# Optimization experiments

Hardware: AMD Instinct MI355X
Metric: run time of the kernel (lower is better)

## Reference

```python
import jax, jax.numpy as jnp
import numpy as np

HEADS, DIM_HEAD, INNER, DIM = 6, 50, 300, 768
HW, EXTRA, POOL = 100, 150, 10  # spatial side, extra tokens, pool output side
N = HW * HW + EXTRA  # 10150


def setup_inputs() -> dict:
    key = jax.random.key(0)
    ks = jax.random.split(key, 6)
    B = 8
    x = jax.random.normal(ks[0], (B, N, DIM), dtype=jnp.float32)
    # weights scaled ~ typical init so softmax logits are sane
    proj_w = jax.random.normal(ks[1], (INNER, DIM), dtype=jnp.float32) * 0.02
    step_x = jax.random.normal(ks[2], (HEADS, 1, 1), dtype=jnp.float32)
    step_rep = jax.random.normal(ks[3], (HEADS, 1, 1), dtype=jnp.float32)
    out_w = jax.random.normal(ks[4], (DIM, INNER), dtype=jnp.float32) * 0.02
    out_b = jax.random.normal(ks[5], (DIM,), dtype=jnp.float32) * 0.02
    return {"x": x, "proj_w": proj_w, "step_x": step_x, "step_rep": step_rep,
            "out_w": out_w, "out_b": out_b}


def reference(x, proj_w, step_x, step_rep, out_w, out_b):
    b, n, c = x.shape
    hw = int(round((n - EXTRA) ** 0.5))
    scale = DIM_HEAD ** -0.5

    w = x @ proj_w.T  # [b, n, 300]

    # adaptive avg pool of the spatial tokens to (10,10); hw % 10 == 0 -> uniform pooling
    k = hw // POOL
    spatial = w[:, : hw * hw, :].reshape(b, hw, hw, INNER).transpose(0, 3, 1, 2)  # [b,300,hw,hw]
    rep = spatial.reshape(b, INNER, POOL, k, POOL, k).mean(axis=(3, 5))  # [b,300,10,10]
    rep = rep.reshape(b, INNER, POOL * POOL).transpose(0, 2, 1)  # [b,100,300]

    wh = w.reshape(b, n, HEADS, DIM_HEAD).transpose(0, 2, 1, 3)        # [b,h,n,d]
    reph = rep.reshape(b, POOL * POOL, HEADS, DIM_HEAD).transpose(0, 2, 1, 3)  # [b,h,100,d]

    # stage 1: rep attends to all tokens
    dots = jnp.einsum('bhqd,bhkd->bhqk', reph, wh) * scale  # [b,h,100,n]
    attn = jax.nn.softmax(dots, axis=-1)
    rep_delta = jnp.einsum('bhqk,bhkd->bhqd', attn, wh)     # [b,h,100,d]
    reph = reph + step_rep * rep_delta

    # stage 2: rep self-attention, broadcast back through reused attn^T
    dots2 = jnp.einsum('bhqd,bhkd->bhqk', reph, reph) * scale  # [b,h,100,100]
    attn2 = jax.nn.softmax(dots2, axis=-1)
    x_delta = jnp.einsum('bhqk,bhkd->bhqd', attn2, reph)       # [b,h,100,d]
    x_delta = jnp.einsum('bhqn,bhqd->bhnd', attn, x_delta)     # attn^T @ x_delta -> [b,h,n,d]
    x_delta = step_x * x_delta

    x_delta = x_delta.transpose(0, 2, 1, 3).reshape(b, n, HEADS * DIM_HEAD)  # [b,n,300]
    return x_delta @ out_w.T + out_b
```

## Files before the change

kernel.cpp:

```cpp
#include <hip/hip_runtime.h>
#include <math.h>

#define BATCH   8
#define NTOK    10150
#define DIMC    768
#define INNERC  300
#define HEADS   6
#define DHEAD   50
#define NQ      100
#define NBH     48
#define NSPLIT  32
#define CHUNK   320
#define SCALE   0.14142135623730951f
#define MTOT    (BATCH*NTOK)
#define XDK     320
#define NEGBIG  -1.0e30f
#define LDS_S   44

typedef __attribute__((ext_vector_type(8))) short short8;
typedef __attribute__((ext_vector_type(4))) float f32x4;

__device__ __forceinline__ ushort f2bf(float x) {
  uint u = __float_as_uint(x);
  uint r = (u + 0x7fffu + ((u >> 16) & 1u)) >> 16;
  return (ushort)r;
}
__device__ __forceinline__ float bf2f(ushort h) {
  return __uint_as_float(((uint)h) << 16);
}

__global__ void split_pad(const float* __restrict__ src, ushort* __restrict__ dHi,
                          ushort* __restrict__ dLo, int R, int C, int Rp, int Cp) {
  const int total = Rp * Cp;
  for (int i = blockIdx.x * blockDim.x + threadIdx.x; i < total;
       i += gridDim.x * blockDim.x) {
    const int r = i / Cp, c = i % Cp;
    const float v = (r < R && c < C) ? src[r * C + c] : 0.f;
    const ushort hh = f2bf(v);
    dHi[i] = hh;
    dLo[i] = f2bf(v - bf2f(hh));
  }
}

__global__ void zero_xd_pad(ushort* __restrict__ xdHi, ushort* __restrict__ xdLo) {
  const int total = MTOT * 20;
  for (int i = blockIdx.x * blockDim.x + threadIdx.x; i < total;
       i += gridDim.x * blockDim.x) {
    const size_t g = (size_t)(i / 20) * XDK + 300 + (i % 20);
    xdHi[g] = 0;
    xdLo[g] = 0;
  }
}

__global__ __launch_bounds__(512, 2) void gemm1_xw(
    const float* __restrict__ x, const ushort* __restrict__ pwHi,
    const ushort* __restrict__ pwLo, ushort* __restrict__ wHi,
    ushort* __restrict__ wLo) {
  __shared__ ushort aH[64][LDS_S], aL[64][LDS_S];
  __shared__ ushort bH[320][LDS_S], bL[320][LDS_S];
  const int t = threadIdx.x;
  const int lane = t & 63, w = t >> 6;
  const int wr = w >> 2, wc = w & 3;
  const int l15 = lane & 15, l4 = lane >> 4;
  const int m0 = blockIdx.x * 64;
  const int arow = t >> 3, aq = (t & 7) * 4;

  f32x4 acc[2][5];
#pragma unroll
  for (int i = 0; i < 2; ++i)
#pragma unroll
    for (int j = 0; j < 5; ++j) acc[i][j] = (f32x4){0.f, 0.f, 0.f, 0.f};

  for (int k0 = 0; k0 < DIMC; k0 += 32) {
    __syncthreads();
    {
      const int m = m0 + arow;
      float4 v = make_float4(0.f, 0.f, 0.f, 0.f);
      if (m < MTOT) v = *(const float4*)&x[(size_t)m * DIMC + k0 + aq];
      ushort h0 = f2bf(v.x), h1 = f2bf(v.y), h2 = f2bf(v.z), h3 = f2bf(v.w);
      *(ushort4*)&aH[arow][aq] = make_ushort4(h0, h1, h2, h3);
      *(ushort4*)&aL[arow][aq] = make_ushort4(
          f2bf(v.x - bf2f(h0)), f2bf(v.y - bf2f(h1)),
          f2bf(v.z - bf2f(h2)), f2bf(v.w - bf2f(h3)));
    }
#pragma unroll
    for (int i = 0; i < 3; ++i) {
      const int sid = t + i * 512;
      if (sid < 1280) {
        const int row = sid >> 2, slot = sid & 3;
        const size_t g = (size_t)row * DIMC + k0 + slot * 8;
        *(short8*)&bH[row][slot * 8] = *(const short8*)&pwHi[g];
        *(short8*)&bL[row][slot * 8] = *(const short8*)&pwLo[g];
      }
    }
    __syncthreads();

    short8 ah[2], al[2];
#pragma unroll
    for (int i = 0; i < 2; ++i) {
      const int row = wr * 32 + i * 16 + l15;
      ah[i] = *(const short8*)&aH[row][l4 * 8];
      al[i] = *(const short8*)&aL[row][l4 * 8];
    }
#pragma unroll
    for (int j = 0; j < 5; ++j) {
      const int brow = wc * 80 + j * 16 + l15;
      const short8 bhf = *(const short8*)&bH[brow][l4 * 8];
      const short8 blf = *(const short8*)&bL[brow][l4 * 8];
#pragma unroll
      for (int i = 0; i < 2; ++i) {
        acc[i][j] = __builtin_amdgcn_mfma_f32_16x16x32_bf16(ah[i], bhf, acc[i][j], 0, 0, 0);
        acc[i][j] = __builtin_amdgcn_mfma_f32_16x16x32_bf16(al[i], bhf, acc[i][j], 0, 0, 0);
        acc[i][j] = __builtin_amdgcn_mfma_f32_16x16x32_bf16(ah[i], blf, acc[i][j], 0, 0, 0);
      }
    }
  }

#pragma unroll
  for (int j = 0; j < 5; ++j) {
    const int col = wc * 80 + j * 16 + l15;
    if (col >= INNERC) continue;
#pragma unroll
    for (int i = 0; i < 2; ++i)
#pragma unroll
      for (int r = 0; r < 4; ++r) {
        const int m = m0 + wr * 32 + i * 16 + l4 * 4 + r;
        if (m < MTOT) {
          const float val = acc[i][j][r];
          const ushort hh = f2bf(val);
          const size_t g = (size_t)m * INNERC + col;
          wHi[g] = hh;
          wLo[g] = f2bf(val - bf2f(hh));
        }
      }
  }
}

__global__ __launch_bounds__(512, 2) void gemm2_out(
    const ushort* __restrict__ xdHi, const ushort* __restrict__ xdLo,
    const ushort* __restrict__ owHi, const ushort* __restrict__ owLo,
    const float* __restrict__ out_b, float* __restrict__ out) {
  __shared__ ushort aH[64][LDS_S], aL[64][LDS_S];
  __shared__ ushort bH[256][LDS_S], bL[256][LDS_S];
  const int t = threadIdx.x;
  const int lane = t & 63, w = t >> 6;
  const int wr = w >> 2, wc = w & 3;
  const int l15 = lane & 15, l4 = lane >> 4;
  const int nwg = gridDim.x;
  const int q = nwg >> 3, r = nwg & 7;
  const int xcd = blockIdx.x & 7, idx = blockIdx.x >> 3;
  const int wg = (xcd < r ? xcd * (q + 1) : r * (q + 1) + (xcd - r) * q) + idx;
  const int bn = wg % 3, bm = wg / 3;
  const int m0 = bm * 64, n0 = bn * 256;
  const int arow = t >> 3, aq = (t & 7) * 4;

  f32x4 acc[2][4];
#pragma unroll
  for (int i = 0; i < 2; ++i)
#pragma unroll
    for (int j = 0; j < 4; ++j) acc[i][j] = (f32x4){0.f, 0.f, 0.f, 0.f};

  for (int k0 = 0; k0 < XDK; k0 += 32) {
    __syncthreads();
    {
      const int m = m0 + arow;
      if (m < MTOT) {
        const size_t g = (size_t)m * XDK + k0 + aq;
        *(ushort4*)&aH[arow][aq] = *(const ushort4*)&xdHi[g];
        *(ushort4*)&aL[arow][aq] = *(const ushort4*)&xdLo[g];
      } else {
        *(ushort4*)&aH[arow][aq] = make_ushort4(0, 0, 0, 0);
        *(ushort4*)&aL[arow][aq] = make_ushort4(0, 0, 0, 0);
      }
    }
#pragma unroll
    for (int i = 0; i < 2; ++i) {
      const int sid = t + i * 512;
      const int row = sid >> 2, slot = sid & 3;
      const size_t g = (size_t)(n0 + row) * XDK + k0 + slot * 8;
      *(short8*)&bH[row][slot * 8] = *(const short8*)&owHi[g];
      *(short8*)&bL[row][slot * 8] = *(const short8*)&owLo[g];
    }
    __syncthreads();

    short8 ah[2], al[2];
#pragma unroll
    for (int i = 0; i < 2; ++i) {
      const int row = wr * 32 + i * 16 + l15;
      ah[i] = *(const short8*)&aH[row][l4 * 8];
      al[i] = *(const short8*)&aL[row][l4 * 8];
    }
#pragma unroll
    for (int j = 0; j < 4; ++j) {
      const int brow = wc * 64 + j * 16 + l15;
      const short8 bhf = *(const short8*)&bH[brow][l4 * 8];
      const short8 blf = *(const short8*)&bL[brow][l4 * 8];
#pragma unroll
      for (int i = 0; i < 2; ++i) {
        acc[i][j] = __builtin_amdgcn_mfma_f32_16x16x32_bf16(ah[i], bhf, acc[i][j], 0, 0, 0);
        acc[i][j] = __builtin_amdgcn_mfma_f32_16x16x32_bf16(al[i], bhf, acc[i][j], 0, 0, 0);
        acc[i][j] = __builtin_amdgcn_mfma_f32_16x16x32_bf16(ah[i], blf, acc[i][j], 0, 0, 0);
      }
    }
  }

#pragma unroll
  for (int j = 0; j < 4; ++j) {
    const int col = n0 + wc * 64 + j * 16 + l15;
    const float bv = out_b[col];
#pragma unroll
    for (int i = 0; i < 2; ++i)
#pragma unroll
      for (int r = 0; r < 4; ++r) {
        const int m = m0 + wr * 32 + i * 16 + l4 * 4 + r;
        if (m < MTOT) out[(size_t)m * DIMC + col] = acc[i][j][r] + bv;
      }
  }
}

__global__ void pool_kernel(const ushort* __restrict__ wHi,
                            const ushort* __restrict__ wLo,
                            float* __restrict__ rep,
                            ushort* __restrict__ repPH, ushort* __restrict__ repPL) {
  int q = blockIdx.x, b = blockIdx.y;
  int i = threadIdx.x;
  if (i < INNERC) {
    int pr = q / 10, pc = q % 10;
    float s = 0.f;
    for (int kr = 0; kr < 10; ++kr)
      for (int kc = 0; kc < 10; ++kc) {
        int tok = (pr * 10 + kr) * 100 + (pc * 10 + kc);
        const size_t g = ((size_t)b * NTOK + tok) * INNERC + i;
        s += bf2f(wHi[g]) + bf2f(wLo[g]);
      }
    s *= 0.01f;
    int h = i / DHEAD, d = i % DHEAD;
    rep[(((size_t)b * HEADS + h) * NQ + q) * DHEAD + d] = s;
    const float sv = s * SCALE;
    const ushort hh = f2bf(sv);
    const size_t pg = (((size_t)b * HEADS + h) * 128 + q) * 64 + d;
    repPH[pg] = hh;
    repPL[pg] = f2bf(sv - bf2f(hh));
  }
  for (int j = threadIdx.x; j < HEADS * 14; j += 320) {
    int h2 = j / 14, d2 = DHEAD + (j % 14);
    const size_t pg = (((size_t)b * HEADS + h2) * 128 + q) * 64 + d2;
    repPH[pg] = 0;
    repPL[pg] = 0;
  }
}

__global__ __launch_bounds__(256, 3) void attn1_mfma(
    const ushort* __restrict__ wHi, const ushort* __restrict__ wLo,
    const float* __restrict__ rep,
    float* __restrict__ m_part, float* __restrict__ l_part,
    float* __restrict__ delta_part) {
  const int bh = blockIdx.x, s = blockIdx.y;
  const int b = bh / HEADS, h = bh % HEADS;
  const int t = threadIdx.x;
  const int lane = t & 63, wv = t >> 6;
  const int l15 = lane & 15, l4 = lane >> 4;

  __shared__ ushort Khi[32][72], Klo[32][72];
  __shared__ ushort VThi[64][40], VTlo[64][40];
  __shared__ ushort Phi[128][40], Plo[128][40];

  short8 qhi[2][2], qlo[2][2];
#pragma unroll
  for (int mi = 0; mi < 2; ++mi) {
#pragma unroll
    for (int ks = 0; ks < 2; ++ks) {
      const int qr = 32 * wv + 16 * mi + l15;
      short8 th, tl;
#pragma unroll
      for (int j = 0; j < 8; ++j) {
        const int k = 32 * ks + 8 * l4 + j;
        float v = (qr < NQ && k < DHEAD)
                      ? rep[((size_t)bh * NQ + qr) * DHEAD + k] * SCALE : 0.f;
        ushort hh = f2bf(v);
        th[j] = (short)hh;
        tl[j] = (short)f2bf(v - bf2f(hh));
      }
      qhi[mi][ks] = th; qlo[mi][ks] = tl;
    }
  }

  f32x4 accO[2][4];
  float m_run[2][4], l_run[2][4];
#pragma unroll
  for (int mi = 0; mi < 2; ++mi) {
#pragma unroll
    for (int r = 0; r < 4; ++r) { m_run[mi][r] = NEGBIG; l_run[mi][r] = 0.f; }
#pragma unroll
    for (int di = 0; di < 4; ++di) accO[mi][di] = (f32x4){0.f, 0.f, 0.f, 0.f};
  }

  const int n0 = s * CHUNK;
  const int n1 = min(NTOK, n0 + CHUNK);

  for (int nt = n0; nt < n1; nt += 32) {
    __syncthreads();
#pragma unroll
    for (int i = 0; i < 4; ++i) {
      const int idx = t + i * 256;
      const int tr = idx >> 5;
      const int d = (idx & 31) * 2;
      const bool inb = (nt + tr < n1) && (d < DHEAD);
      uint hv = 0, lv = 0;
      if (inb) {
        const size_t g = ((size_t)b * NTOK + nt + tr) * INNERC + h * DHEAD + d;
        hv = *(const uint*)&wHi[g];
        lv = *(const uint*)&wLo[g];
      }
      *(uint*)&Khi[tr][d] = hv;
      *(uint*)&Klo[tr][d] = lv;
      const int ps = ((((tr >> 3) + (d >> 3)) & 3) << 3) + (tr & 7);
      VThi[d][ps] = (ushort)(hv & 0xffffu);
      VTlo[d][ps] = (ushort)(lv & 0xffffu);
      VThi[d + 1][ps] = (ushort)(hv >> 16);
      VTlo[d + 1][ps] = (ushort)(lv >> 16);
    }
    __syncthreads();

    f32x4 accS[2][2];
#pragma unroll
    for (int mi = 0; mi < 2; ++mi)
#pragma unroll
      for (int ni = 0; ni < 2; ++ni) accS[mi][ni] = (f32x4){0.f, 0.f, 0.f, 0.f};
#pragma unroll
    for (int ks = 0; ks < 2; ++ks) {
      short8 kh[2], kl[2];
#pragma unroll
      for (int ni = 0; ni < 2; ++ni) {
        kh[ni] = *(const short8*)&Khi[16 * ni + l15][32 * ks + 8 * l4];
        kl[ni] = *(const short8*)&Klo[16 * ni + l15][32 * ks + 8 * l4];
      }
#pragma unroll
      for (int mi = 0; mi < 2; ++mi)
#pragma unroll
        for (int ni = 0; ni < 2; ++ni) {
          accS[mi][ni] = __builtin_amdgcn_mfma_f32_16x16x32_bf16(qhi[mi][ks], kh[ni], accS[mi][ni], 0, 0, 0);
          accS[mi][ni] = __builtin_amdgcn_mfma_f32_16x16x32_bf16(qlo[mi][ks], kh[ni], accS[mi][ni], 0, 0, 0);
          accS[mi][ni] = __builtin_amdgcn_mfma_f32_16x16x32_bf16(qhi[mi][ks], kl[ni], accS[mi][ni], 0, 0, 0);
        }
    }

    bool cval[2];
#pragma unroll
    for (int ni = 0; ni < 2; ++ni) cval[ni] = (nt + 16 * ni + l15) < n1;
#pragma unroll
    for (int mi = 0; mi < 2; ++mi) {
#pragma unroll
      for (int ni = 0; ni < 2; ++ni)
        if (!cval[ni]) {
#pragma unroll
          for (int r = 0; r < 4; ++r) accS[mi][ni][r] = NEGBIG;
        }
#pragma unroll
      for (int r = 0; r < 4; ++r) {
        float mx = fmaxf(accS[mi][0][r], accS[mi][1][r]);
        mx = fmaxf(mx, __shfl_xor(mx, 1));
        mx = fmaxf(mx, __shfl_xor(mx, 2));
        mx = fmaxf(mx, __shfl_xor(mx, 4));
        mx = fmaxf(mx, __shfl_xor(mx, 8));
        const float m_new = fmaxf(m_run[mi][r], mx);
        const float sc = __expf(m_run[mi][r] - m_new);
        m_run[mi][r] = m_new;
        l_run[mi][r] *= sc;
#pragma unroll
        for (int di = 0; di < 4; ++di) accO[mi][di][r] *= sc;
        float ps = 0.f;
#pragma unroll
        for (int ni = 0; ni < 2; ++ni) {
          const float p = __expf(accS[mi][ni][r] - m_new);
          accS[mi][ni][r] = p;
          ps += p;
        }
        ps += __shfl_xor(ps, 1);
        ps += __shfl_xor(ps, 2);
        ps += __shfl_xor(ps, 4);
        ps += __shfl_xor(ps, 8);
        l_run[mi][r] += ps;
      }
#pragma unroll
      for (int ni = 0; ni < 2; ++ni)
#pragma unroll
        for (int r = 0; r < 4; ++r) {
          const int row = 32 * wv + 16 * mi + 4 * l4 + r;
          const int col = 16 * ni + l15;
          const float p = accS[mi][ni][r];
          const ushort ph = f2bf(p);
          Phi[row][col] = ph;
          Plo[row][col] = f2bf(p - bf2f(ph));
        }
    }

#pragma unroll
    for (int mi = 0; mi < 2; ++mi) {
      const short8 pah = *(const short8*)&Phi[32 * wv + 16 * mi + l15][8 * l4];
      const short8 pal = *(const short8*)&Plo[32 * wv + 16 * mi + l15][8 * l4];
#pragma unroll
      for (int di = 0; di < 4; ++di) {
        const int vs = (((l4 + 2 * di + (l15 >> 3)) & 3)) << 3;
        const short8 vbh = *(const short8*)&VThi[16 * di + l15][vs];
        const short8 vbl = *(const short8*)&VTlo[16 * di + l15][vs];
        accO[mi][di] = __builtin_amdgcn_mfma_f32_16x16x32_bf16(pah, vbh, accO[mi][di], 0, 0, 0);
        accO[mi][di] = __builtin_amdgcn_mfma_f32_16x16x32_bf16(pal, vbh, accO[mi][di], 0, 0, 0);
        accO[mi][di] = __builtin_amdgcn_mfma_f32_16x16x32_bf16(pah, vbl, accO[mi][di], 0, 0, 0);
      }
    }
  }

  const size_t base = ((size_t)bh * NSPLIT + s) * NQ;
#pragma unroll
  for (int mi = 0; mi < 2; ++mi)
#pragma unroll
    for (int r = 0; r < 4; ++r) {
      const int q = 32 * wv + 16 * mi + 4 * l4 + r;
      if (q < NQ && l15 == 0) {
        m_part[base + q] = m_run[mi][r];
        l_part[base + q] = l_run[mi][r];
      }
#pragma unroll
      for (int di = 0; di < 4; ++di) {
        const int d = 16 * di + l15;
        if (q < NQ && d < DHEAD)
          delta_part[(base + q) * DHEAD + d] = accO[mi][di][r];
      }
    }
}

__global__ __launch_bounds__(256) void attn1_combine(
    const float* __restrict__ rep, const float* __restrict__ m_part,
    const float* __restrict__ l_part, const float* __restrict__ delta_part,
    const float* __restrict__ step_rep,
    float* __restrict__ reph2, float* __restrict__ m_fin, float* __restrict__ l_fin) {
  int bh = blockIdx.x;
  int h = bh % HEADS;
  int t = threadIdx.x;
  __shared__ float Mf[NQ], Lf[NQ];
  if (t < NQ) {
    int q = t;
    float M = -INFINITY;
#pragma unroll
    for (int s2 = 0; s2 < NSPLIT; ++s2)
      M = fmaxf(M, m_part[((size_t)bh * NSPLIT + s2) * NQ + q]);
    float L = 0.f;
#pragma unroll
    for (int s2 = 0; s2 < NSPLIT; ++s2)
      L += l_part[((size_t)bh * NSPLIT + s2) * NQ + q] *
           __expf(m_part[((size_t)bh * NSPLIT + s2) * NQ + q] - M);
    Mf[q] = M; Lf[q] = L;
    m_fin[(size_t)bh * NQ + q] = M;
    l_fin[(size_t)bh * NQ + q] = L;
  }
  __syncthreads();
  float sr = step_rep[h];
  for (int idx = t; idx < NQ * DHEAD; idx += 256) {
    int q = idx / DHEAD, d = idx % DHEAD;
    float sum = 0.f;
#pragma unroll
    for (int s2 = 0; s2 < NSPLIT; ++s2) {
      size_t pb = ((size_t)bh * NSPLIT + s2) * NQ + q;
      sum += __expf(m_part[pb] - Mf[q]) * delta_part[pb * DHEAD + d];
    }
    float rd = sum / Lf[q];
    reph2[(size_t)bh * NQ * DHEAD + idx] =
        rep[(size_t)bh * NQ * DHEAD + idx] + sr * rd;
  }
}

__global__ __launch_bounds__(256) void attn2_kernel(
    const float* __restrict__ reph2, const float* __restrict__ step_x,
    ushort* __restrict__ xqTH, ushort* __restrict__ xqTL) {
  int bh = blockIdx.x;
  int h = bh % HEADS;
  int t = threadIdx.x;
  __shared__ float r2[NQ * DHEAD];
  __shared__ float att[NQ * NQ];

  for (int idx = t; idx < NQ * DHEAD; idx += 256)
    r2[idx] = reph2[(size_t)bh * NQ * DHEAD + idx];
  __syncthreads();

  for (int idx = t; idx < NQ * NQ; idx += 256) {
    int qq = idx / NQ, jj = idx % NQ;
    float s = 0.f;
#pragma unroll
    for (int k = 0; k < DHEAD; ++k) s += r2[qq * DHEAD + k] * r2[jj * DHEAD + k];
    att[idx] = s * SCALE;
  }
  __syncthreads();
  if (t < NQ) {
    float M = -INFINITY;
    for (int j = 0; j < NQ; ++j) M = fmaxf(M, att[t * NQ + j]);
    float L = 0.f;
    for (int j = 0; j < NQ; ++j) { float e = __expf(att[t * NQ + j] - M); att[t * NQ + j] = e; L += e; }
    float inv = 1.f / L;
    for (int j = 0; j < NQ; ++j) att[t * NQ + j] *= inv;
  }
  __syncthreads();
  float sx = step_x[h];
  for (int idx = t; idx < NQ * DHEAD; idx += 256) {
    int qd_q = idx / DHEAD, d = idx % DHEAD;
    float v = 0.f;
#pragma unroll
    for (int j = 0; j < NQ; ++j) v += att[qd_q * NQ + j] * r2[j * DHEAD + d];
    v *= sx;
    const size_t pg = ((size_t)bh * 64 + d) * 128 + qd_q;
    const ushort hh = f2bf(v);
    xqTH[pg] = hh;
    xqTL[pg] = f2bf(v - bf2f(hh));
  }
  for (int idx = t; idx < 64 * 28; idx += 256) {
    int d = idx / 28, qq2 = NQ + (idx % 28);
    const size_t pg = ((size_t)bh * 64 + d) * 128 + qq2;
    xqTH[pg] = 0;
    xqTL[pg] = 0;
  }
}

#define TT5 128
__global__ __launch_bounds__(256, 2) void bcast5_kernel(
    const ushort* __restrict__ wHi, const ushort* __restrict__ wLo,
    const ushort* __restrict__ repPH, const ushort* __restrict__ repPL,
    const ushort* __restrict__ xqTH, const ushort* __restrict__ xqTL,
    const float* __restrict__ m_fin, const float* __restrict__ l_fin,
    ushort* __restrict__ xdHi, ushort* __restrict__ xdLo) {
  const int tile = blockIdx.x, bh = blockIdx.y;
  const int b = bh / HEADS, h = bh % HEADS;
  const int tok0 = tile * TT5;
  const int t = threadIdx.x;
  const int lane = t & 63, wv = t >> 6;
  const int l15 = lane & 15, l4 = lane >> 4;

  __shared__ ushort pH[128][72], pL[128][72];

  short8 awh[2][2], awl[2][2];
#pragma unroll
  for (int st = 0; st < 2; ++st) {
    const int tokA = tok0 + st * 64 + 16 * wv + l15;
#pragma unroll
    for (int ks = 0; ks < 2; ++ks) {
      const int kbase = 32 * ks + 8 * l4;
      uint hv[4] = {0, 0, 0, 0}, lv[4] = {0, 0, 0, 0};
      if (tokA < NTOK && kbase < DHEAD) {
        const size_t g = ((size_t)b * NTOK + tokA) * INNERC + h * DHEAD + kbase;
#pragma unroll
        for (int c = 0; c < 4; ++c) {
          hv[c] = *(const uint*)&wHi[g + 2 * c];
          lv[c] = *(const uint*)&wLo[g + 2 * c];
        }
      }
      short8 th, tl;
#pragma unroll
      for (int j = 0; j < 8; ++j) {
        const bool ok = (kbase + j) < DHEAD;
        const ushort hsel = (j & 1) ? (ushort)(hv[j >> 1] >> 16) : (ushort)(hv[j >> 1] & 0xffffu);
        const ushort lsel = (j & 1) ? (ushort)(lv[j >> 1] >> 16) : (ushort)(lv[j >> 1] & 0xffffu);
        th[j] = ok ? (short)hsel : (short)0;
        tl[j] = ok ? (short)lsel : (short)0;
      }
      awh[st][ks] = th;
      awl[st][ks] = tl;
    }
  }

  f32x4 accO[2][4];
#pragma unroll
  for (int st = 0; st < 2; ++st)
#pragma unroll
    for (int di = 0; di < 4; ++di) accO[st][di] = (f32x4){0.f, 0.f, 0.f, 0.f};

#pragma unroll
  for (int qc = 0; qc < 2; ++qc) {
    const int q0 = qc * 64;

    short8 rbh[4][2], rbl[4][2];
#pragma unroll
    for (int ni = 0; ni < 4; ++ni)
#pragma unroll
      for (int ks = 0; ks < 2; ++ks) {
        const size_t rg = (((size_t)bh * 128) + (q0 + 16 * ni + l15)) * 64 + 32 * ks + 8 * l4;
        rbh[ni][ks] = *(const short8*)&repPH[rg];
        rbl[ni][ks] = *(const short8*)&repPL[rg];
      }
    float mq[4], li[4];
    bool vq[4];
#pragma unroll
    for (int ni = 0; ni < 4; ++ni) {
      const int q = q0 + 16 * ni + l15;
      vq[ni] = (q < NQ);
      mq[ni] = vq[ni] ? m_fin[(size_t)bh * NQ + q] : 0.f;
      li[ni] = vq[ni] ? 1.f / l_fin[(size_t)bh * NQ + q] : 0.f;
    }

#pragma unroll
    for (int st = 0; st < 2; ++st) {
      f32x4 accS[4];
#pragma unroll
      for (int ni = 0; ni < 4; ++ni) accS[ni] = (f32x4){0.f, 0.f, 0.f, 0.f};
#pragma unroll
      for (int ks = 0; ks < 2; ++ks)
#pragma unroll
        for (int ni = 0; ni < 4; ++ni) {
          accS[ni] = __builtin_amdgcn_mfma_f32_16x16x32_bf16(awh[st][ks], rbh[ni][ks], accS[ni], 0, 0, 0);
          accS[ni] = __builtin_amdgcn_mfma_f32_16x16x32_bf16(awl[st][ks], rbh[ni][ks], accS[ni], 0, 0, 0);
          accS[ni] = __builtin_amdgcn_mfma_f32_16x16x32_bf16(awh[st][ks], rbl[ni][ks], accS[ni], 0, 0, 0);
        }
#pragma unroll
      for (int ni = 0; ni < 4; ++ni) {
#pragma unroll
        for (int r = 0; r < 4; ++r) {
          const float p = vq[ni] ? __expf(accS[ni][r] - mq[ni]) * li[ni] : 0.f;
          const int row = st * 64 + 16 * wv + 4 * l4 + r;
          const ushort ph = f2bf(p);
          pH[row][16 * ni + l15] = ph;
          pL[row][16 * ni + l15] = f2bf(p - bf2f(ph));
        }
      }
    }

    short8 xbh[4][2], xbl[4][2];
#pragma unroll
    for (int di = 0; di < 4; ++di)
#pragma unroll
      for (int ks2 = 0; ks2 < 2; ++ks2) {
        const size_t xg = (((size_t)bh * 64) + (16 * di + l15)) * 128 + q0 + 32 * ks2 + 8 * l4;
        xbh[di][ks2] = *(const short8*)&xqTH[xg];
        xbl[di][ks2] = *(const short8*)&xqTL[xg];
      }

#pragma unroll
    for (int st = 0; st < 2; ++st) {
#pragma unroll
      for (int ks2 = 0; ks2 < 2; ++ks2) {
        const short8 pah = *(const short8*)&pH[st * 64 + 16 * wv + l15][32 * ks2 + 8 * l4];
        const short8 pal = *(const short8*)&pL[st * 64 + 16 * wv + l15][32 * ks2 + 8 * l4];
#pragma unroll
        for (int di = 0; di < 4; ++di) {
          accO[st][di] = __builtin_amdgcn_mfma_f32_16x16x32_bf16(pah, xbh[di][ks2], accO[st][di], 0, 0, 0);
          accO[st][di] = __builtin_amdgcn_mfma_f32_16x16x32_bf16(pal, xbh[di][ks2], accO[st][di], 0, 0, 0);
          accO[st][di] = __builtin_amdgcn_mfma_f32_16x16x32_bf16(pah, xbl[di][ks2], accO[st][di], 0, 0, 0);
        }
      }
    }
  }

#pragma unroll
  for (int st = 0; st < 2; ++st)
#pragma unroll
    for (int di = 0; di < 4; ++di) {
      const int d = di * 16 + l15;
      if (d >= DHEAD) continue;
#pragma unroll
      for (int r = 0; r < 4; ++r) {
        const int tok = tok0 + st * 64 + wv * 16 + 4 * l4 + r;
        if (tok < NTOK) {
          const float val = accO[st][di][r];
          const ushort hh = f2bf(val);
          const size_t g = ((size_t)b * NTOK + tok) * XDK + h * DHEAD + d;
          xdHi[g] = hh;
          xdLo[g] = f2bf(val - bf2f(hh));
        }
      }
    }
}

extern "C" void kernel_launch(void* const* d_in, const int* in_sizes, int n_in,
                              void* d_out, int out_size, void* d_ws, size_t ws_size,
                              hipStream_t stream) {
  const float* x        = (const float*)d_in[0];
  const float* proj_w   = (const float*)d_in[1];
  const float* step_x   = (const float*)d_in[2];
  const float* step_rep = (const float*)d_in[3];
  const float* out_w    = (const float*)d_in[4];
  const float* out_b    = (const float*)d_in[5];
  float* out = (float*)d_out;

  uint8_t* p8 = (uint8_t*)d_ws;
  ushort* wHi    = (ushort*)(p8);
  ushort* wLo    = (ushort*)(p8 + 48720000);
  float*  rep    = (float*) (p8 + 97440000);
  float*  reph2  = (float*) (p8 + 98400000);
  float*  m_part = (float*) (p8 + 100320000);
  float*  l_part = (float*) (p8 + 100934400);
  float*  m_fin  = (float*) (p8 + 101548800);
  float*  l_fin  = (float*) (p8 + 101568000);
  ushort* xdHi   = (ushort*)(p8 + 101587200);
  ushort* xdLo   = (ushort*)(p8 + 153555200);
  ushort* pwHi   = (ushort*)(p8 + 205523200);
  ushort* pwLo   = (ushort*)(p8 + 206014720);
  ushort* owHi   = (ushort*)(p8 + 206506240);
  ushort* owLo   = (ushort*)(p8 + 206997760);
  ushort* repPH  = (ushort*)(p8 + 207489280);
  ushort* repPL  = (ushort*)(p8 + 208275712);
  ushort* xqTH   = (ushort*)(p8 + 209062144);
  ushort* xqTL   = (ushort*)(p8 + 209848576);
  float* delta = (float*)xdHi;

  split_pad<<<960, 256, 0, stream>>>(proj_w, pwHi, pwLo, INNERC, DIMC, 320, DIMC);
  split_pad<<<960, 256, 0, stream>>>(out_w, owHi, owLo, DIMC, INNERC, DIMC, XDK);
  gemm1_xw<<<1269, 512, 0, stream>>>(x, pwHi, pwLo, wHi, wLo);
  pool_kernel<<<dim3(NQ, BATCH), 320, 0, stream>>>(wHi, wLo, rep, repPH, repPL);
  attn1_mfma<<<dim3(NBH, NSPLIT), 256, 0, stream>>>(wHi, wLo, rep, m_part, l_part, delta);
  attn1_combine<<<NBH, 256, 0, stream>>>(rep, m_part, l_part, delta, step_rep,
                                         reph2, m_fin, l_fin);
  zero_xd_pad<<<2048, 256, 0, stream>>>(xdHi, xdLo);
  attn2_kernel<<<NBH, 256, 0, stream>>>(reph2, step_x, xqTH, xqTL);
  bcast5_kernel<<<dim3(80, NBH), 256, 0, stream>>>(
      wHi, wLo, repPH, repPL, xqTH, xqTL, m_fin, l_fin, xdHi, xdLo);
  gemm2_out<<<3807, 512, 0, stream>>>(xdHi, xdLo, owHi, owLo, out_b, out);
}
```

Measured before the change: 778.4 us.

## Drop LDS staging in both GEMMs and load MFMA fragments directly from global

```diff
diff --git a/kernel.cpp b/kernel.cpp
--- a/kernel.cpp
+++ b/kernel.cpp
@@ -15,7 +15,6 @@
 #define MTOT    (BATCH*NTOK)
 #define XDK     320
 #define NEGBIG  -1.0e30f
-#define LDS_S   44
 
 typedef __attribute__((ext_vector_type(8))) short short8;
 typedef __attribute__((ext_vector_type(4))) float f32x4;
@@ -52,18 +51,15 @@
   }
 }
 
-__global__ __launch_bounds__(512, 2) void gemm1_xw(
+__global__ __launch_bounds__(512, 3) void gemm1_xw(
     const float* __restrict__ x, const ushort* __restrict__ pwHi,
     const ushort* __restrict__ pwLo, ushort* __restrict__ wHi,
     ushort* __restrict__ wLo) {
-  __shared__ ushort aH[64][LDS_S], aL[64][LDS_S];
-  __shared__ ushort bH[320][LDS_S], bL[320][LDS_S];
   const int t = threadIdx.x;
   const int lane = t & 63, w = t >> 6;
   const int wr = w >> 2, wc = w & 3;
   const int l15 = lane & 15, l4 = lane >> 4;
   const int m0 = blockIdx.x * 64;
-  const int arow = t >> 3, aq = (t & 7) * 4;
 
   f32x4 acc[2][5];
 #pragma unroll
@@ -71,47 +67,56 @@
 #pragma unroll
     for (int j = 0; j < 5; ++j) acc[i][j] = (f32x4){0.f, 0.f, 0.f, 0.f};
 
-  for (int k0 = 0; k0 < DIMC; k0 += 32) {
-    __syncthreads();
-    {
-      const int m = m0 + arow;
-      float4 v = make_float4(0.f, 0.f, 0.f, 0.f);
-      if (m < MTOT) v = *(const float4*)&x[(size_t)m * DIMC + k0 + aq];
-      ushort h0 = f2bf(v.x), h1 = f2bf(v.y), h2 = f2bf(v.z), h3 = f2bf(v.w);
-      *(ushort4*)&aH[arow][aq] = make_ushort4(h0, h1, h2, h3);
-      *(ushort4*)&aL[arow][aq] = make_ushort4(
-          f2bf(v.x - bf2f(h0)), f2bf(v.y - bf2f(h1)),
-          f2bf(v.z - bf2f(h2)), f2bf(v.w - bf2f(h3)));
-    }
-#pragma unroll
-    for (int i = 0; i < 3; ++i) {
-      const int sid = t + i * 512;
-      if (sid < 1280) {
-        const int row = sid >> 2, slot = sid & 3;
-        const size_t g = (size_t)row * DIMC + k0 + slot * 8;
-        *(short8*)&bH[row][slot * 8] = *(const short8*)&pwHi[g];
-        *(short8*)&bL[row][slot * 8] = *(const short8*)&pwLo[g];
-      }
-    }
-    __syncthreads();
-
-    short8 ah[2], al[2];
-#pragma unroll
-    for (int i = 0; i < 2; ++i) {
-      const int row = wr * 32 + i * 16 + l15;
-      ah[i] = *(const short8*)&aH[row][l4 * 8];
-      al[i] = *(const short8*)&aL[row][l4 * 8];
-    }
+  int mrow[2];
+  bool mok[2];
+#pragma unroll
+  for (int i = 0; i < 2; ++i) {
+    mrow[i] = m0 + wr * 32 + i * 16 + l15;
+    mok[i] = mrow[i] < MTOT;
+  }
+
+  for (int k0 = 0; k0 < DIMC; k0 += 64) {
+    short8 ah[2][2], al[2][2];
+#pragma unroll
+    for (int i = 0; i < 2; ++i)
+#pragma unroll
+      for (int ks = 0; ks < 2; ++ks) {
+        float v[8];
+        if (mok[i]) {
+          const float* p = &x[(size_t)mrow[i] * DIMC + k0 + ks * 32 + l4 * 8];
+          const float4 u0 = *(const float4*)p;
+          const float4 u1 = *(const float4*)(p + 4);
+          v[0] = u0.x; v[1] = u0.y; v[2] = u0.z; v[3] = u0.w;
+          v[4] = u1.x; v[5] = u1.y; v[6] = u1.z; v[7] = u1.w;
+        } else {
+#pragma unroll
+          for (int jj = 0; jj < 8; ++jj) v[jj] = 0.f;
+        }
+        short8 th, tl;
+#pragma unroll
+        for (int jj = 0; jj < 8; ++jj) {
+          const ushort hh = f2bf(v[jj]);
+          th[jj] = (short)hh;
+          tl[jj] = (short)f2bf(v[jj] - bf2f(hh));
+        }
+        ah[i][ks] = th;
+        al[i][ks] = tl;
+      }
+
 #pragma unroll
     for (int j = 0; j < 5; ++j) {
       const int brow = wc * 80 + j * 16 + l15;
-      const short8 bhf = *(const short8*)&bH[brow][l4 * 8];
-      const short8 blf = *(const short8*)&bL[brow][l4 * 8];
-#pragma unroll
-      for (int i = 0; i < 2; ++i) {
-        acc[i][j] = __builtin_amdgcn_mfma_f32_16x16x32_bf16(ah[i], bhf, acc[i][j], 0, 0, 0);
-        acc[i][j] = __builtin_amdgcn_mfma_f32_16x16x32_bf16(al[i], bhf, acc[i][j], 0, 0, 0);
-        acc[i][j] = __builtin_amdgcn_mfma_f32_16x16x32_bf16(ah[i], blf, acc[i][j], 0, 0, 0);
+#pragma unroll
+      for (int ks = 0; ks < 2; ++ks) {
+        const size_t g = (size_t)brow * DIMC + k0 + ks * 32 + l4 * 8;
+        const short8 bhf = *(const short8*)&pwHi[g];
+        const short8 blf = *(const short8*)&pwLo[g];
+#pragma unroll
+        for (int i = 0; i < 2; ++i) {
+          acc[i][j] = __builtin_amdgcn_mfma_f32_16x16x32_bf16(ah[i][ks], bhf, acc[i][j], 0, 0, 0);
+          acc[i][j] = __builtin_amdgcn_mfma_f32_16x16x32_bf16(al[i][ks], bhf, acc[i][j], 0, 0, 0);
+          acc[i][j] = __builtin_amdgcn_mfma_f32_16x16x32_bf16(ah[i][ks], blf, acc[i][j], 0, 0, 0);
+        }
       }
     }
   }
@@ -136,12 +141,10 @@
   }
 }
 
-__global__ __launch_bounds__(512, 2) void gemm2_out(
+__global__ __launch_bounds__(512, 3) void gemm2_out(
     const ushort* __restrict__ xdHi, const ushort* __restrict__ xdLo,
     const ushort* __restrict__ owHi, const ushort* __restrict__ owLo,
     const float* __restrict__ out_b, float* __restrict__ out) {
-  __shared__ ushort aH[64][LDS_S], aL[64][LDS_S];
-  __shared__ ushort bH[256][LDS_S], bL[256][LDS_S];
   const int t = threadIdx.x;
   const int lane = t & 63, w = t >> 6;
   const int wr = w >> 2, wc = w & 3;
@@ -152,7 +155,6 @@
   const int wg = (xcd < r ? xcd * (q + 1) : r * (q + 1) + (xcd - r) * q) + idx;
   const int bn = wg % 3, bm = wg / 3;
   const int m0 = bm * 64, n0 = bn * 256;
-  const int arow = t >> 3, aq = (t & 7) * 4;
 
   f32x4 acc[2][4];
 #pragma unroll
@@ -160,46 +162,45 @@
 #pragma unroll
     for (int j = 0; j < 4; ++j) acc[i][j] = (f32x4){0.f, 0.f, 0.f, 0.f};
 
-  for (int k0 = 0; k0 < XDK; k0 += 32) {
-    __syncthreads();
-    {
-      const int m = m0 + arow;
-      if (m < MTOT) {
-        const size_t g = (size_t)m * XDK + k0 + aq;
-        *(ushort4*)&aH[arow][aq] = *(const ushort4*)&xdHi[g];
-        *(ushort4*)&aL[arow][aq] = *(const ushort4*)&xdLo[g];
-      } else {
-        *(ushort4*)&aH[arow][aq] = make_ushort4(0, 0, 0, 0);
-        *(ushort4*)&aL[arow][aq] = make_ushort4(0, 0, 0, 0);
-      }
-    }
-#pragma unroll
-    for (int i = 0; i < 2; ++i) {
-      const int sid = t + i * 512;
-      const int row = sid >> 2, slot = sid & 3;
-      const size_t g = (size_t)(n0 + row) * XDK + k0 + slot * 8;
-      *(short8*)&bH[row][slot * 8] = *(const short8*)&owHi[g];
-      *(short8*)&bL[row][slot * 8] = *(const short8*)&owLo[g];
-    }
-    __syncthreads();
-
-    short8 ah[2], al[2];
-#pragma unroll
-    for (int i = 0; i < 2; ++i) {
-      const int row = wr * 32 + i * 16 + l15;
-      ah[i] = *(const short8*)&aH[row][l4 * 8];
-      al[i] = *(const short8*)&aL[row][l4 * 8];
-    }
+  int mrow[2];
+  bool mok[2];
+#pragma unroll
+  for (int i = 0; i < 2; ++i) {
+    mrow[i] = m0 + wr * 32 + i * 16 + l15;
+    mok[i] = mrow[i] < MTOT;
+  }
+
+  for (int k0 = 0; k0 < XDK; k0 += 64) {
+    short8 ah[2][2], al[2][2];
+#pragma unroll
+    for (int i = 0; i < 2; ++i)
+#pragma unroll
+      for (int ks = 0; ks < 2; ++ks) {
+        if (mok[i]) {
+          const size_t g = (size_t)mrow[i] * XDK + k0 + ks * 32 + l4 * 8;
+          ah[i][ks] = *(const short8*)&xdHi[g];
+          al[i][ks] = *(const short8*)&xdLo[g];
+        } else {
+          const short8 z = {0, 0, 0, 0, 0, 0, 0, 0};
+          ah[i][ks] = z;
+          al[i][ks] = z;
+        }
+      }
+
 #pragma unroll
     for (int j = 0; j < 4; ++j) {
-      const int brow = wc * 64 + j * 16 + l15;
-      const short8 bhf = *(const short8*)&bH[brow][l4 * 8];
-      const short8 blf = *(const short8*)&bL[brow][l4 * 8];
-#pragma unroll
-      for (int i = 0; i < 2; ++i) {
-        acc[i][j] = __builtin_amdgcn_mfma_f32_16x16x32_bf16(ah[i], bhf, acc[i][j], 0, 0, 0);
-        acc[i][j] = __builtin_amdgcn_mfma_f32_16x16x32_bf16(al[i], bhf, acc[i][j], 0, 0, 0);
-        acc[i][j] = __builtin_amdgcn_mfma_f32_16x16x32_bf16(ah[i], blf, acc[i][j], 0, 0, 0);
+      const int brow = n0 + wc * 64 + j * 16 + l15;
+#pragma unroll
+      for (int ks = 0; ks < 2; ++ks) {
+        const size_t g = (size_t)brow * XDK + k0 + ks * 32 + l4 * 8;
+        const short8 bhf = *(const short8*)&owHi[g];
+        const short8 blf = *(const short8*)&owLo[g];
+#pragma unroll
+        for (int i = 0; i < 2; ++i) {
+          acc[i][j] = __builtin_amdgcn_mfma_f32_16x16x32_bf16(ah[i][ks], bhf, acc[i][j], 0, 0, 0);
+          acc[i][j] = __builtin_amdgcn_mfma_f32_16x16x32_bf16(al[i][ks], bhf, acc[i][j], 0, 0, 0);
+          acc[i][j] = __builtin_amdgcn_mfma_f32_16x16x32_bf16(ah[i][ks], blf, acc[i][j], 0, 0, 0);
+        }
       }
     }
   }
```

Result: slower. 1.249 ms (+60.5%).
